# Kernel tuning notes

Hardware: AMD Instinct MI355X
Metric: run time of the kernel (lower is better)

Reference implementation:

```python
import jax, jax.numpy as jnp
from jax import lax
import numpy as np

N, T, D_OBS, D_Z, D_U = 32, 1024, 128, 64, 8
H_ENC, H_BW, H_DYN = 256, 128, 256
D_A = 2 * D_Z  # natural-parameter dim (mean-part, precision-part)


def setup_inputs() -> dict:
    key = jax.random.key(0)
    ks = jax.random.split(key, 16)

    def w(k, shape):
        return (jax.random.normal(k, shape, jnp.float32) / np.sqrt(shape[0]).astype(np.float32))

    return {
        "t": jnp.broadcast_to(jnp.arange(T, dtype=jnp.int32), (N, T)),
        "y": jax.random.normal(ks[0], (N, T, D_OBS), jnp.float32),
        "u": 0.1 * jax.random.normal(ks[1], (N, T, D_U), jnp.float32),
        "enc_w1": w(ks[2], (D_OBS, H_ENC)),
        "enc_b1": jnp.zeros((H_ENC,), jnp.float32),
        "enc_w2": w(ks[3], (H_ENC, D_A)),
        "enc_b2": jnp.zeros((D_A,), jnp.float32),
        "bw_wa": w(ks[4], (D_A, H_BW)),
        "bw_wh": w(ks[5], (H_BW, H_BW)),
        "bw_b": jnp.zeros((H_BW,), jnp.float32),
        "bw_wo": w(ks[6], (H_BW, D_A)),
        "bw_bo": jnp.zeros((D_A,), jnp.float32),
        "dyn_w1": w(ks[7], (D_Z + D_U, H_DYN)),
        "dyn_b1": jnp.zeros((H_DYN,), jnp.float32),
        "dyn_w2": w(ks[8], (H_DYN, D_Z)),
        "dyn_b2": jnp.zeros((D_Z,), jnp.float32),
        "q_raw": 0.1 * jax.random.normal(ks[9], (D_Z,), jnp.float32),
        "m0": jnp.zeros((D_Z,), jnp.float32),
        "v0": jnp.ones((D_Z,), jnp.float32),
    }


def _constrain_natural(nat):
    # DiagMVN: first half is the mean-natural-param, second half must be <= 0
    e1, e2 = nat[..., :D_Z], nat[..., D_Z:]
    return jnp.concatenate([e1, -jax.nn.softplus(e2)], axis=-1)


def reference(t, y, u, enc_w1, enc_b1, enc_w2, enc_b2,
              bw_wa, bw_wh, bw_b, bw_wo, bw_bo,
              dyn_w1, dyn_b1, dyn_w2, dyn_b2, q_raw, m0, v0):
    # --- local obs encoder (per-step MLP), dropout prob = 0.0 so mask == 1 ---
    h = jnp.tanh(jnp.einsum('ntd,dh->nth', y, enc_w1) + enc_b1)
    a = jnp.einsum('nth,ha->nta', h, enc_w2) + enc_b2          # [N,T,2Dz]

    # --- backward encoder: reverse recurrence over time (pseudo mode) ---
    a_t = jnp.swapaxes(a, 0, 1)                                # [T,N,2Dz]

    def bw_step(h_next, a_step):
        hcell = jnp.tanh(a_step @ bw_wa + h_next @ bw_wh + bw_b)
        return hcell, hcell @ bw_wo + bw_bo

    _, b_t = lax.scan(bw_step, jnp.zeros((N, H_BW), a.dtype), a_t, reverse=True)
    alpha = _constrain_natural(b_t)                            # [T,N,2Dz]

    # --- vmap'd sequential natural-parameter filter over time ---
    Q = jax.nn.softplus(q_raw)                                 # diag state noise
    u_t = jnp.swapaxes(u, 0, 1)                                # [T,N,Du]

    def step(carry, xs):
        m, v = carry
        alpha_step, u_step = xs
        x = jnp.concatenate([m, u_step], axis=-1)
        m_p = jnp.tanh(x @ dyn_w1 + dyn_b1) @ dyn_w2 + dyn_b2  # predictive mean
        v_p = v + Q                                            # predictive var
        e1 = m_p / v_p + alpha_step[..., :D_Z]
        e2 = -0.5 / v_p + alpha_step[..., D_Z:]                # stays < 0
        v_s = -0.5 / e2
        m_s = v_s * e1
        return (m_s, v_s), (jnp.concatenate([m_s, v_s], -1),
                            jnp.concatenate([m_p, v_p], -1))

    m_init = jnp.broadcast_to(m0, (N, D_Z))
    v_init = jnp.broadcast_to(v0, (N, D_Z))
    _, (moment_s, moment_p) = lax.scan(step, (m_init, v_init), (alpha, u_t))

    out = jnp.concatenate([moment_s, moment_p], axis=-1)       # [T,N,4Dz]
    return jnp.swapaxes(out, 0, 1)                             # [N,T,4Dz]
```

## Files before the change

### kernel.cpp

```cpp
#include <hip/hip_runtime.h>
#include <math.h>

#define T_LEN 1024
#define NB 32

typedef _Float16 h2 __attribute__((ext_vector_type(2)));

__device__ __forceinline__ h2 f2h2(float f) { return __builtin_bit_cast(h2, f); }

__device__ __forceinline__ float dot2(h2 a, h2 b, float c) {
#if __has_builtin(__builtin_amdgcn_fdot2)
    return __builtin_amdgcn_fdot2(a, b, c, false);
#else
    return fmaf((float)a[0], (float)b[0], fmaf((float)a[1], (float)b[1], c));
#endif
}

#define DPP_ADD(v, ctrl) do { \
    int _xi = __builtin_bit_cast(int, v); \
    int _yi = __builtin_amdgcn_update_dpp(_xi, _xi, (ctrl), 0xF, 0xF, true); \
    v += __builtin_bit_cast(float, _yi); } while (0)

__device__ __forceinline__ float softplus_f(float x) {
    return fmaxf(x, 0.f) + log1pf(expf(-fabsf(x)));
}

__device__ __forceinline__ float fast_tanh(float x) {
    float e = __builtin_amdgcn_exp2f(x * 2.88539008177792681472f);
    float r = __builtin_amdgcn_rcpf(1.f + e);
    return 1.f - 2.f * r;
}

__device__ __forceinline__ void bar_sync() {
    asm volatile("s_waitcnt lgkmcnt(0)" ::: "memory");
    __builtin_amdgcn_s_barrier();
    asm volatile("" ::: "memory");
}

__global__ __launch_bounds__(256) void k_encoder(
    const float* __restrict__ y, const float* __restrict__ u,
    const float* __restrict__ w1, const float* __restrict__ b1,
    const float* __restrict__ w2, const float* __restrict__ b2,
    const float* __restrict__ wa, const float* __restrict__ bb,
    const float* __restrict__ dynw1, const float* __restrict__ dynb1,
    float* __restrict__ apre, float* __restrict__ preU)
{
    __shared__ float ly[8][128];
    __shared__ float lh[8][256];
    __shared__ float la[8][128];
    __shared__ float lu[8][8];
    const int tid = threadIdx.x;
    const int row0 = blockIdx.x * 8;

    ((float4*)&ly[0][0])[tid] = ((const float4*)(y + (size_t)row0 * 128))[tid];
    if (tid < 16)
        ((float4*)&lu[0][0])[tid] = ((const float4*)(u + (size_t)row0 * 8))[tid];
    __syncthreads();

    {
        float acc[8] = {0,0,0,0,0,0,0,0};
        for (int i = 0; i < 128; i += 4) {
            float w0 = w1[(i+0)*256 + tid];
            float w1v = w1[(i+1)*256 + tid];
            float w2v = w1[(i+2)*256 + tid];
            float w3 = w1[(i+3)*256 + tid];
            #pragma unroll
            for (int r = 0; r < 8; ++r) {
                float4 yv = *(const float4*)&ly[r][i];
                acc[r] += yv.x*w0 + yv.y*w1v + yv.z*w2v + yv.w*w3;
            }
        }
        float bias = b1[tid];
        #pragma unroll
        for (int r = 0; r < 8; ++r) lh[r][tid] = fast_tanh(acc[r] + bias);
    }
    __syncthreads();

    {
        const int d = tid & 127, rh = tid >> 7;
        float acc[4] = {0,0,0,0};
        for (int i = 0; i < 256; i += 4) {
            float w0 = w2[(i+0)*128 + d];
            float w1v = w2[(i+1)*128 + d];
            float w2v = w2[(i+2)*128 + d];
            float w3 = w2[(i+3)*128 + d];
            #pragma unroll
            for (int q = 0; q < 4; ++q) {
                float4 hv = *(const float4*)&lh[rh*4+q][i];
                acc[q] += hv.x*w0 + hv.y*w1v + hv.z*w2v + hv.w*w3;
            }
        }
        float bias = b2[d];
        #pragma unroll
        for (int q = 0; q < 4; ++q) la[rh*4+q][d] = acc[q] + bias;
    }
    __syncthreads();

    {
        const int j = tid & 127, rh = tid >> 7;
        float acc[4] = {0,0,0,0};
        for (int i = 0; i < 128; i += 4) {
            float w0 = wa[(i+0)*128 + j];
            float w1v = wa[(i+1)*128 + j];
            float w2v = wa[(i+2)*128 + j];
            float w3 = wa[(i+3)*128 + j];
            #pragma unroll
            for (int q = 0; q < 4; ++q) {
                float4 av = *(const float4*)&la[rh*4+q][i];
                acc[q] += av.x*w0 + av.y*w1v + av.z*w2v + av.w*w3;
            }
        }
        float bias = bb[j];
        #pragma unroll
        for (int q = 0; q < 4; ++q) {
            int rn = row0 + rh*4 + q;
            int n = rn >> 10, t = rn & 1023;
            apre[((size_t)t*NB + n)*128 + j] = acc[q] + bias;
        }
    }

    {
        float wu[8];
        #pragma unroll
        for (int c = 0; c < 8; ++c) wu[c] = dynw1[(64 + c)*256 + tid];
        float bias = dynb1[tid];
        #pragma unroll
        for (int r = 0; r < 8; ++r) {
            float acc = bias;
            #pragma unroll
            for (int c = 0; c < 8; ++c) acc += lu[r][c] * wu[c];
            int rn = row0 + r;
            int n = rn >> 10, t = rn & 1023;
            preU[((size_t)t*NB + n)*256 + tid] = acc;
        }
    }
}

__global__ __launch_bounds__(1024, 1) void k_bwscan(
    const float* __restrict__ apre, const float* __restrict__ wh,
    float* __restrict__ hcell)
{
    const int n = blockIdx.x;
    const int tid = threadIdx.x;
    const int j = tid >> 3, p = tid & 7;
    __shared__ _Float16 h[2][128];

    h2 w0, w1, w2, w3, w4, w5, w6, w7;
    {
        const float* s = wh + (size_t)(p * 16) * 128 + j;
        w0 = h2{(_Float16)s[0*128],  (_Float16)s[1*128]};
        w1 = h2{(_Float16)s[2*128],  (_Float16)s[3*128]};
        w2 = h2{(_Float16)s[4*128],  (_Float16)s[5*128]};
        w3 = h2{(_Float16)s[6*128],  (_Float16)s[7*128]};
        w4 = h2{(_Float16)s[8*128],  (_Float16)s[9*128]};
        w5 = h2{(_Float16)s[10*128], (_Float16)s[11*128]};
        w6 = h2{(_Float16)s[12*128], (_Float16)s[13*128]};
        w7 = h2{(_Float16)s[14*128], (_Float16)s[15*128]};
    }

    if (tid < 128) h[0][tid] = (_Float16)0.f;
    __syncthreads();

    float apA = apre[((size_t)1023*NB + n)*128 + j];
    float apB = apre[((size_t)1022*NB + n)*128 + j];

#define BWSTEP(cur, nxt, apv, tt) do { \
        const _Float16* hb = &h[cur][p*16]; \
        float4 r0 = *(const float4*)hb; \
        float4 r1 = *(const float4*)(hb + 8); \
        float c0 = dot2(f2h2(r0.x), w0, 0.f); \
        float c1 = dot2(f2h2(r0.y), w1, 0.f); \
        float c2 = dot2(f2h2(r0.z), w2, 0.f); \
        float c3 = dot2(f2h2(r0.w), w3, 0.f); \
        c0 = dot2(f2h2(r1.x), w4, c0); \
        c1 = dot2(f2h2(r1.y), w5, c1); \
        c2 = dot2(f2h2(r1.z), w6, c2); \
        c3 = dot2(f2h2(r1.w), w7, c3); \
        float acc = (c0+c1) + (c2+c3); \
        DPP_ADD(acc, 0xB1); \
        DPP_ADD(acc, 0x4E); \
        DPP_ADD(acc, 0x141); \
        float hc = fast_tanh(acc + apv); \
        if (p == 0) h[nxt][j] = (_Float16)hc; \
        else if (p == 1) hcell[((size_t)(tt)*NB + n)*128 + j] = hc; \
        bar_sync(); } while (0)

    for (int t = 1023; t > 0; t -= 2) {
        float apN0 = 0.f, apN1 = 0.f;
        if (t - 2 >= 0) apN0 = apre[((size_t)(t-2)*NB + n)*128 + j];
        BWSTEP(0, 1, apA, t);
        if (t - 3 >= 0) apN1 = apre[((size_t)(t-3)*NB + n)*128 + j];
        BWSTEP(1, 0, apB, t - 1);
        apA = apN0; apB = apN1;
    }
#undef BWSTEP
}

__global__ __launch_bounds__(256) void k_alpha(
    const float* __restrict__ hcell, const float* __restrict__ wo,
    const float* __restrict__ bo, float* __restrict__ alpha)
{
    __shared__ float lhc[8][128];
    const int tid = threadIdx.x;
    const size_t base = (size_t)blockIdx.x * 8 * 128;
    ((float4*)&lhc[0][0])[tid] = ((const float4*)(hcell + base))[tid];
    __syncthreads();

    const int j = tid & 127, rh = tid >> 7;
    float acc[4] = {0,0,0,0};
    for (int i = 0; i < 128; i += 4) {
        float w0 = wo[(i+0)*128 + j];
        float w1v = wo[(i+1)*128 + j];
        float w2v = wo[(i+2)*128 + j];
        float w3 = wo[(i+3)*128 + j];
        #pragma unroll
        for (int q = 0; q < 4; ++q) {
            float4 hv = *(const float4*)&lhc[rh*4+q][i];
            acc[q] += hv.x*w0 + hv.y*w1v + hv.z*w2v + hv.w*w3;
        }
    }
    float bias = bo[j];
    const int dpos = (j & 63) * 2 + (j >> 6);
    #pragma unroll
    for (int q = 0; q < 4; ++q) {
        float b = acc[q] + bias;
        float val = (j < 64) ? b : -softplus_f(b);
        alpha[base + (size_t)(rh*4+q)*128 + dpos] = val;
    }
}

#define LHF(x) ((x) + (((x) >> 4) << 3))

__global__ __launch_bounds__(1024, 1) void k_fwscan(
    const float* __restrict__ alpha, const float* __restrict__ preU,
    const float* __restrict__ dynw1, const float* __restrict__ dynw2,
    const float* __restrict__ dynb2, const float* __restrict__ qraw,
    const float* __restrict__ m0, const float* __restrict__ v0,
    float* __restrict__ out)
{
    const int n = blockIdx.x;
    const int tid = threadIdx.x;
    const int hh = tid >> 2, pp = tid & 3;
    const int d2 = (tid >> 3) & 63, qq = tid & 7;
    const bool lowhalf = (tid < 512);
    __shared__ _Float16 lm[2][64];
    __shared__ _Float16 lhid[384];

    h2 u0, u1, u2, u3, u4, u5, u6, u7;
    {
        const float* s = dynw1 + (size_t)(pp * 16) * 256 + hh;
        u0 = h2{(_Float16)s[0*256], (_Float16)s[1*256]};
        u1 = h2{(_Float16)s[2*256], (_Float16)s[3*256]};
        u2 = h2{(_Float16)s[4*256], (_Float16)s[5*256]};
        u3 = h2{(_Float16)s[6*256], (_Float16)s[7*256]};
        u4 = h2{(_Float16)s[8*256], (_Float16)s[9*256]};
        u5 = h2{(_Float16)s[10*256], (_Float16)s[11*256]};
        u6 = h2{(_Float16)s[12*256], (_Float16)s[13*256]};
        u7 = h2{(_Float16)s[14*256], (_Float16)s[15*256]};
    }
    h2 v0p, v1p, v2p, v3p, v4p, v5p, v6p, v7p;
    h2 v8p, v9p, vap, vbp, vcp, vdp, vep, vfp;
    {
        const float* s = dynw2 + (size_t)(qq * 32) * 64 + d2;
        v0p = h2{(_Float16)s[0*64],  (_Float16)s[1*64]};
        v1p = h2{(_Float16)s[2*64],  (_Float16)s[3*64]};
        v2p = h2{(_Float16)s[4*64],  (_Float16)s[5*64]};
        v3p = h2{(_Float16)s[6*64],  (_Float16)s[7*64]};
        v4p = h2{(_Float16)s[8*64],  (_Float16)s[9*64]};
        v5p = h2{(_Float16)s[10*64], (_Float16)s[11*64]};
        v6p = h2{(_Float16)s[12*64], (_Float16)s[13*64]};
        v7p = h2{(_Float16)s[14*64], (_Float16)s[15*64]};
        v8p = h2{(_Float16)s[16*64], (_Float16)s[17*64]};
        v9p = h2{(_Float16)s[18*64], (_Float16)s[19*64]};
        vap = h2{(_Float16)s[20*64], (_Float16)s[21*64]};
        vbp = h2{(_Float16)s[22*64], (_Float16)s[23*64]};
        vcp = h2{(_Float16)s[24*64], (_Float16)s[25*64]};
        vdp = h2{(_Float16)s[26*64], (_Float16)s[27*64]};
        vep = h2{(_Float16)s[28*64], (_Float16)s[29*64]};
        vfp = h2{(_Float16)s[30*64], (_Float16)s[31*64]};
    }

    const float Qv  = softplus_f(qraw[d2]);
    const float b2v = dynb2[d2];
    float vreg = v0[d2];
    if (tid < 64) lm[0][tid] = (_Float16)m0[tid];

    float hp0 = preU[(size_t)n * 256 + hh];
    float hp1 = preU[((size_t)NB + n)*256 + hh];
    float2 av0 = make_float2(0.f, 0.f), av1 = make_float2(0.f, 0.f);
    if (lowhalf) {
        av0 = *(const float2*)&alpha[(size_t)n * 128 + d2*2];
        av1 = *(const float2*)&alpha[((size_t)NB + n)*128 + d2*2];
    }
    __syncthreads();

    int cur = 0;
    for (int t = 0; t < T_LEN; ++t) {
        float hpN = 0.f;
        float2 avN = make_float2(0.f, 0.f);
        if (t + 2 < T_LEN) {
            hpN = preU[((size_t)(t+2)*NB + n)*256 + hh];
            if (lowhalf)
                avN = *(const float2*)&alpha[((size_t)(t+2)*NB + n)*128 + d2*2];
        }

        {
            const _Float16* mb = &lm[cur][pp*16];
            float4 r0 = *(const float4*)mb;
            float4 r1 = *(const float4*)(mb + 8);
            float c0 = dot2(f2h2(r0.x), u0, 0.f);
            float c1 = dot2(f2h2(r0.y), u1, 0.f);
            float c2 = dot2(f2h2(r0.z), u2, 0.f);
            float c3 = dot2(f2h2(r0.w), u3, 0.f);
            c0 = dot2(f2h2(r1.x), u4, c0);
            c1 = dot2(f2h2(r1.y), u5, c1);
            c2 = dot2(f2h2(r1.z), u6, c2);
            c3 = dot2(f2h2(r1.w), u7, c3);
            float acc = (c0+c1) + (c2+c3);
            DPP_ADD(acc, 0xB1);
            DPP_ADD(acc, 0x4E);
            if (pp == 0) lhid[LHF(hh)] = (_Float16)fast_tanh(hp0 + acc);
        }
        bar_sync();

        if (lowhalf) {
            const _Float16* hbA = &lhid[LHF(qq*32)];
            const _Float16* hbB = &lhid[LHF(qq*32 + 16)];
            float4 r0 = *(const float4*)hbA;
            float4 r1 = *(const float4*)(hbA + 8);
            float4 r2 = *(const float4*)hbB;
            float4 r3 = *(const float4*)(hbB + 8);
            float c0 = dot2(f2h2(r0.x), v0p, 0.f);
            float c1 = dot2(f2h2(r0.y), v1p, 0.f);
            float c2 = dot2(f2h2(r0.z), v2p, 0.f);
            float c3 = dot2(f2h2(r0.w), v3p, 0.f);
            c0 = dot2(f2h2(r1.x), v4p, c0);
            c1 = dot2(f2h2(r1.y), v5p, c1);
            c2 = dot2(f2h2(r1.z), v6p, c2);
            c3 = dot2(f2h2(r1.w), v7p, c3);
            c0 = dot2(f2h2(r2.x), v8p, c0);
            c1 = dot2(f2h2(r2.y), v9p, c1);
            c2 = dot2(f2h2(r2.z), vap, c2);
            c3 = dot2(f2h2(r2.w), vbp, c3);
            c0 = dot2(f2h2(r3.x), vcp, c0);
            c1 = dot2(f2h2(r3.y), vdp, c1);
            c2 = dot2(f2h2(r3.z), vep, c2);
            c3 = dot2(f2h2(r3.w), vfp, c3);
            float acc = (c0+c1) + (c2+c3);
            DPP_ADD(acc, 0xB1);
            DPP_ADD(acc, 0x4E);
            DPP_ADD(acc, 0x141);

            float m_p = acc + b2v;
            float v_p = vreg + Qv;
            float rvp = __builtin_amdgcn_rcpf(v_p);
            float e1 = m_p * rvp + av0.x;
            float e2 = av0.y - 0.5f * rvp;
            float v_s = -0.5f * __builtin_amdgcn_rcpf(e2);
            float m_s = v_s * e1;
            vreg = v_s;
            if (qq == 0) lm[cur ^ 1][d2] = (_Float16)m_s;

            if (qq < 4) {
                size_t ob = ((size_t)n * T_LEN + t) * 256;
                float val = (qq == 0) ? m_s : (qq == 1) ? v_s : (qq == 2) ? m_p : v_p;
                out[ob + (size_t)qq*64 + d2] = val;
            }
        }
        bar_sync();
        cur ^= 1;
        hp0 = hp1; hp1 = hpN;
        av0 = av1; av1 = avN;
    }
}

extern "C" void kernel_launch(void* const* d_in, const int* in_sizes, int n_in,
                              void* d_out, int out_size, void* d_ws, size_t ws_size,
                              hipStream_t stream) {
    const float* y      = (const float*)d_in[1];
    const float* u      = (const float*)d_in[2];
    const float* enc_w1 = (const float*)d_in[3];
    const float* enc_b1 = (const float*)d_in[4];
    const float* enc_w2 = (const float*)d_in[5];
    const float* enc_b2 = (const float*)d_in[6];
    const float* bw_wa  = (const float*)d_in[7];
    const float* bw_wh  = (const float*)d_in[8];
    const float* bw_b   = (const float*)d_in[9];
    const float* bw_wo  = (const float*)d_in[10];
    const float* bw_bo  = (const float*)d_in[11];
    const float* dyn_w1 = (const float*)d_in[12];
    const float* dyn_b1 = (const float*)d_in[13];
    const float* dyn_w2 = (const float*)d_in[14];
    const float* dyn_b2 = (const float*)d_in[15];
    const float* q_raw  = (const float*)d_in[16];
    const float* m0     = (const float*)d_in[17];
    const float* v0     = (const float*)d_in[18];
    float* out = (float*)d_out;

    float* ws = (float*)d_ws;
    float* apre  = ws;
    float* hcell = ws + 4194304;
    float* alpha = ws;
    float* preU  = ws + 2 * 4194304;

    k_encoder<<<4096, 256, 0, stream>>>(y, u, enc_w1, enc_b1, enc_w2, enc_b2,
                                        bw_wa, bw_b, dyn_w1, dyn_b1, apre, preU);
    k_bwscan<<<NB, 1024, 0, stream>>>(apre, bw_wh, hcell);
    k_alpha<<<4096, 256, 0, stream>>>(hcell, bw_wo, bw_bo, alpha);
    k_fwscan<<<NB, 1024, 0, stream>>>(alpha, preU, dyn_w1, dyn_w2, dyn_b2,
                                      q_raw, m0, v0, out);
}
```

Before: 1.245 ms.

## Shrink scan blocks to 256 threads with more per-thread dot-product work

Both recurrent scan kernels (backward encoder and forward filter) now launch 256 threads per sequence instead of 1024. Each thread keeps 64-element weight slices in registers and does longer dot products, so fewer DPP cross-lane reduction steps are needed and the per-step barrier spans 4 waves instead of 16. The cost is a longer serial dot-product chain per thread and higher register pressure on each step of the latency-bound scan.

```diff
diff --git a/kernel.cpp b/kernel.cpp
--- a/kernel.cpp
+++ b/kernel.cpp
@@ -136,26 +136,21 @@
     }
 }
 
-__global__ __launch_bounds__(1024, 1) void k_bwscan(
+__global__ __launch_bounds__(256, 1) void k_bwscan(
     const float* __restrict__ apre, const float* __restrict__ wh,
     float* __restrict__ hcell)
 {
     const int n = blockIdx.x;
     const int tid = threadIdx.x;
-    const int j = tid >> 3, p = tid & 7;
+    const int j = tid >> 1, p = tid & 1;
     __shared__ _Float16 h[2][128];
 
-    h2 w0, w1, w2, w3, w4, w5, w6, w7;
-    {
-        const float* s = wh + (size_t)(p * 16) * 128 + j;
-        w0 = h2{(_Float16)s[0*128],  (_Float16)s[1*128]};
-        w1 = h2{(_Float16)s[2*128],  (_Float16)s[3*128]};
-        w2 = h2{(_Float16)s[4*128],  (_Float16)s[5*128]};
-        w3 = h2{(_Float16)s[6*128],  (_Float16)s[7*128]};
-        w4 = h2{(_Float16)s[8*128],  (_Float16)s[9*128]};
-        w5 = h2{(_Float16)s[10*128], (_Float16)s[11*128]};
-        w6 = h2{(_Float16)s[12*128], (_Float16)s[13*128]};
-        w7 = h2{(_Float16)s[14*128], (_Float16)s[15*128]};
+    h2 w[32];
+    {
+        const float* s = wh + (size_t)(p * 64) * 128 + j;
+        #pragma unroll
+        for (int k = 0; k < 32; ++k)
+            w[k] = h2{(_Float16)s[(2*k)*128], (_Float16)s[(2*k+1)*128]};
     }
 
     if (tid < 128) h[0][tid] = (_Float16)0.f;
@@ -165,24 +160,23 @@
     float apB = apre[((size_t)1022*NB + n)*128 + j];
 
 #define BWSTEP(cur, nxt, apv, tt) do { \
-        const _Float16* hb = &h[cur][p*16]; \
-        float4 r0 = *(const float4*)hb; \
-        float4 r1 = *(const float4*)(hb + 8); \
-        float c0 = dot2(f2h2(r0.x), w0, 0.f); \
-        float c1 = dot2(f2h2(r0.y), w1, 0.f); \
-        float c2 = dot2(f2h2(r0.z), w2, 0.f); \
-        float c3 = dot2(f2h2(r0.w), w3, 0.f); \
-        c0 = dot2(f2h2(r1.x), w4, c0); \
-        c1 = dot2(f2h2(r1.y), w5, c1); \
-        c2 = dot2(f2h2(r1.z), w6, c2); \
-        c3 = dot2(f2h2(r1.w), w7, c3); \
+        const _Float16* hb = &h[cur][p*64]; \
+        float4 mr[8]; \
+        _Pragma("unroll") \
+        for (int k = 0; k < 8; ++k) mr[k] = ((const float4*)hb)[k]; \
+        float c0 = 0.f, c1 = 0.f, c2 = 0.f, c3 = 0.f; \
+        _Pragma("unroll") \
+        for (int k = 0; k < 8; ++k) { \
+            c0 = dot2(f2h2(mr[k].x), w[4*k+0], c0); \
+            c1 = dot2(f2h2(mr[k].y), w[4*k+1], c1); \
+            c2 = dot2(f2h2(mr[k].z), w[4*k+2], c2); \
+            c3 = dot2(f2h2(mr[k].w), w[4*k+3], c3); \
+        } \
         float acc = (c0+c1) + (c2+c3); \
         DPP_ADD(acc, 0xB1); \
-        DPP_ADD(acc, 0x4E); \
-        DPP_ADD(acc, 0x141); \
         float hc = fast_tanh(acc + apv); \
         if (p == 0) h[nxt][j] = (_Float16)hc; \
-        else if (p == 1) hcell[((size_t)(tt)*NB + n)*128 + j] = hc; \
+        else        hcell[((size_t)(tt)*NB + n)*128 + j] = hc; \
         bar_sync(); } while (0)
 
     for (int t = 1023; t > 0; t -= 2) {
@@ -231,7 +225,7 @@
 
 #define LHF(x) ((x) + (((x) >> 4) << 3))
 
-__global__ __launch_bounds__(1024, 1) void k_fwscan(
+__global__ __launch_bounds__(256, 1) void k_fwscan(
     const float* __restrict__ alpha, const float* __restrict__ preU,
     const float* __restrict__ dynw1, const float* __restrict__ dynw2,
     const float* __restrict__ dynb2, const float* __restrict__ qraw,
@@ -240,44 +234,24 @@
 {
     const int n = blockIdx.x;
     const int tid = threadIdx.x;
-    const int hh = tid >> 2, pp = tid & 3;
-    const int d2 = (tid >> 3) & 63, qq = tid & 7;
-    const bool lowhalf = (tid < 512);
+    const int hh = tid;
+    const int d2 = tid >> 2, qq = tid & 3;
     __shared__ _Float16 lm[2][64];
     __shared__ _Float16 lhid[384];
 
-    h2 u0, u1, u2, u3, u4, u5, u6, u7;
-    {
-        const float* s = dynw1 + (size_t)(pp * 16) * 256 + hh;
-        u0 = h2{(_Float16)s[0*256], (_Float16)s[1*256]};
-        u1 = h2{(_Float16)s[2*256], (_Float16)s[3*256]};
-        u2 = h2{(_Float16)s[4*256], (_Float16)s[5*256]};
-        u3 = h2{(_Float16)s[6*256], (_Float16)s[7*256]};
-        u4 = h2{(_Float16)s[8*256], (_Float16)s[9*256]};
-        u5 = h2{(_Float16)s[10*256], (_Float16)s[11*256]};
-        u6 = h2{(_Float16)s[12*256], (_Float16)s[13*256]};
-        u7 = h2{(_Float16)s[14*256], (_Float16)s[15*256]};
-    }
-    h2 v0p, v1p, v2p, v3p, v4p, v5p, v6p, v7p;
-    h2 v8p, v9p, vap, vbp, vcp, vdp, vep, vfp;
-    {
-        const float* s = dynw2 + (size_t)(qq * 32) * 64 + d2;
-        v0p = h2{(_Float16)s[0*64],  (_Float16)s[1*64]};
-        v1p = h2{(_Float16)s[2*64],  (_Float16)s[3*64]};
-        v2p = h2{(_Float16)s[4*64],  (_Float16)s[5*64]};
-        v3p = h2{(_Float16)s[6*64],  (_Float16)s[7*64]};
-        v4p = h2{(_Float16)s[8*64],  (_Float16)s[9*64]};
-        v5p = h2{(_Float16)s[10*64], (_Float16)s[11*64]};
-        v6p = h2{(_Float16)s[12*64], (_Float16)s[13*64]};
-        v7p = h2{(_Float16)s[14*64], (_Float16)s[15*64]};
-        v8p = h2{(_Float16)s[16*64], (_Float16)s[17*64]};
-        v9p = h2{(_Float16)s[18*64], (_Float16)s[19*64]};
-        vap = h2{(_Float16)s[20*64], (_Float16)s[21*64]};
-        vbp = h2{(_Float16)s[22*64], (_Float16)s[23*64]};
-        vcp = h2{(_Float16)s[24*64], (_Float16)s[25*64]};
-        vdp = h2{(_Float16)s[26*64], (_Float16)s[27*64]};
-        vep = h2{(_Float16)s[28*64], (_Float16)s[29*64]};
-        vfp = h2{(_Float16)s[30*64], (_Float16)s[31*64]};
+    h2 u[32];
+    {
+        const float* s = dynw1 + hh;
+        #pragma unroll
+        for (int k = 0; k < 32; ++k)
+            u[k] = h2{(_Float16)s[(2*k)*256], (_Float16)s[(2*k+1)*256]};
+    }
+    h2 v[32];
+    {
+        const float* s = dynw2 + (size_t)(qq * 64) * 64 + d2;
+        #pragma unroll
+        for (int k = 0; k < 32; ++k)
+            v[k] = h2{(_Float16)s[(2*k)*64], (_Float16)s[(2*k+1)*64]};
     }
 
     const float Qv  = softplus_f(qraw[d2]);
@@ -287,11 +261,8 @@
 
     float hp0 = preU[(size_t)n * 256 + hh];
     float hp1 = preU[((size_t)NB + n)*256 + hh];
-    float2 av0 = make_float2(0.f, 0.f), av1 = make_float2(0.f, 0.f);
-    if (lowhalf) {
-        av0 = *(const float2*)&alpha[(size_t)n * 128 + d2*2];
-        av1 = *(const float2*)&alpha[((size_t)NB + n)*128 + d2*2];
-    }
+    float2 av0 = *(const float2*)&alpha[(size_t)n * 128 + d2*2];
+    float2 av1 = *(const float2*)&alpha[((size_t)NB + n)*128 + d2*2];
     __syncthreads();
 
     int cur = 0;
@@ -300,56 +271,46 @@
         float2 avN = make_float2(0.f, 0.f);
         if (t + 2 < T_LEN) {
             hpN = preU[((size_t)(t+2)*NB + n)*256 + hh];
-            if (lowhalf)
-                avN = *(const float2*)&alpha[((size_t)(t+2)*NB + n)*128 + d2*2];
+            avN = *(const float2*)&alpha[((size_t)(t+2)*NB + n)*128 + d2*2];
         }
 
         {
-            const _Float16* mb = &lm[cur][pp*16];
-            float4 r0 = *(const float4*)mb;
-            float4 r1 = *(const float4*)(mb + 8);
-            float c0 = dot2(f2h2(r0.x), u0, 0.f);
-            float c1 = dot2(f2h2(r0.y), u1, 0.f);
-            float c2 = dot2(f2h2(r0.z), u2, 0.f);
-            float c3 = dot2(f2h2(r0.w), u3, 0.f);
-            c0 = dot2(f2h2(r1.x), u4, c0);
-            c1 = dot2(f2h2(r1.y), u5, c1);
-            c2 = dot2(f2h2(r1.z), u6, c2);
-            c3 = dot2(f2h2(r1.w), u7, c3);
+            const _Float16* mb = &lm[cur][0];
+            float4 mr[8];
+            #pragma unroll
+            for (int k = 0; k < 8; ++k) mr[k] = ((const float4*)mb)[k];
+            float c0 = 0.f, c1 = 0.f, c2 = 0.f, c3 = 0.f;
+            #pragma unroll
+            for (int k = 0; k < 8; ++k) {
+                c0 = dot2(f2h2(mr[k].x), u[4*k+0], c0);
+                c1 = dot2(f2h2(mr[k].y), u[4*k+1], c1);
+                c2 = dot2(f2h2(mr[k].z), u[4*k+2], c2);
+                c3 = dot2(f2h2(mr[k].w), u[4*k+3], c3);
+            }
+            float acc = (c0+c1) + (c2+c3);
+            lhid[LHF(hh)] = (_Float16)fast_tanh(hp0 + acc);
+        }
+        bar_sync();
+
+        {
+            float4 hr[8];
+            #pragma unroll
+            for (int c = 0; c < 4; ++c) {
+                const _Float16* hb = &lhid[LHF(qq*64 + 16*c)];
+                hr[2*c+0] = ((const float4*)hb)[0];
+                hr[2*c+1] = ((const float4*)hb)[1];
+            }
+            float c0 = 0.f, c1 = 0.f, c2 = 0.f, c3 = 0.f;
+            #pragma unroll
+            for (int k = 0; k < 8; ++k) {
+                c0 = dot2(f2h2(hr[k].x), v[4*k+0], c0);
+                c1 = dot2(f2h2(hr[k].y), v[4*k+1], c1);
+                c2 = dot2(f2h2(hr[k].z), v[4*k+2], c2);
+                c3 = dot2(f2h2(hr[k].w), v[4*k+3], c3);
+            }
             float acc = (c0+c1) + (c2+c3);
             DPP_ADD(acc, 0xB1);
             DPP_ADD(acc, 0x4E);
-            if (pp == 0) lhid[LHF(hh)] = (_Float16)fast_tanh(hp0 + acc);
-        }
-        bar_sync();
-
-        if (lowhalf) {
-            const _Float16* hbA = &lhid[LHF(qq*32)];
-            const _Float16* hbB = &lhid[LHF(qq*32 + 16)];
-            float4 r0 = *(const float4*)hbA;
-            float4 r1 = *(const float4*)(hbA + 8);
-            float4 r2 = *(const float4*)hbB;
-            float4 r3 = *(const float4*)(hbB + 8);
-            float c0 = dot2(f2h2(r0.x), v0p, 0.f);
-            float c1 = dot2(f2h2(r0.y), v1p, 0.f);
-            float c2 = dot2(f2h2(r0.z), v2p, 0.f);
-            float c3 = dot2(f2h2(r0.w), v3p, 0.f);
-            c0 = dot2(f2h2(r1.x), v4p, c0);
-            c1 = dot2(f2h2(r1.y), v5p, c1);
-            c2 = dot2(f2h2(r1.z), v6p, c2);
-            c3 = dot2(f2h2(r1.w), v7p, c3);
-            c0 = dot2(f2h2(r2.x), v8p, c0);
-            c1 = dot2(f2h2(r2.y), v9p, c1);
-            c2 = dot2(f2h2(r2.z), vap, c2);
-            c3 = dot2(f2h2(r2.w), vbp, c3);
-            c0 = dot2(f2h2(r3.x), vcp, c0);
-            c1 = dot2(f2h2(r3.y), vdp, c1);
-            c2 = dot2(f2h2(r3.z), vep, c2);
-            c3 = dot2(f2h2(r3.w), vfp, c3);
-            float acc = (c0+c1) + (c2+c3);
-            DPP_ADD(acc, 0xB1);
-            DPP_ADD(acc, 0x4E);
-            DPP_ADD(acc, 0x141);
 
             float m_p = acc + b2v;
             float v_p = vreg + Qv;
@@ -361,11 +322,9 @@
             vreg = v_s;
             if (qq == 0) lm[cur ^ 1][d2] = (_Float16)m_s;
 
-            if (qq < 4) {
-                size_t ob = ((size_t)n * T_LEN + t) * 256;
-                float val = (qq == 0) ? m_s : (qq == 1) ? v_s : (qq == 2) ? m_p : v_p;
-                out[ob + (size_t)qq*64 + d2] = val;
-            }
+            size_t ob = ((size_t)n * T_LEN + t) * 256;
+            float val = (qq == 0) ? m_s : (qq == 1) ? v_s : (qq == 2) ? m_p : v_p;
+            out[ob + (size_t)qq*64 + d2] = val;
         }
         bar_sync();
         cur ^= 1;
@@ -405,8 +364,8 @@
 
     k_encoder<<<4096, 256, 0, stream>>>(y, u, enc_w1, enc_b1, enc_w2, enc_b2,
                                         bw_wa, bw_b, dyn_w1, dyn_b1, apre, preU);
-    k_bwscan<<<NB, 1024, 0, stream>>>(apre, bw_wh, hcell);
+    k_bwscan<<<NB, 256, 0, stream>>>(apre, bw_wh, hcell);
     k_alpha<<<4096, 256, 0, stream>>>(hcell, bw_wo, bw_bo, alpha);
-    k_fwscan<<<NB, 1024, 0, stream>>>(alpha, preU, dyn_w1, dyn_w2, dyn_b2,
-                                      q_raw, m0, v0, out);
-}
+    k_fwscan<<<NB, 256, 0, stream>>>(alpha, preU, dyn_w1, dyn_w2, dyn_b2,
+                                     q_raw, m0, v0, out);
+}
```

Measured after the change: 1.115 ms. 1.12x faster.
